# Performance work log

Measured on AMD Instinct MI355X. Metric: run time of the kernel, lower is better.

## Reference

```python
import jax, jax.numpy as jnp
import numpy as np
from jax import lax

DN = ('NCHW', 'OIHW', 'NCHW')
K = 7  # kernel_size


def _conv(x, w, pad):
    return lax.conv_general_dilated(x, w, (1, 1), pad, dimension_numbers=DN)


def _rgb2gray(im):
    if im.shape[1] == 3:
        w = jnp.array([0.299, 0.587, 0.114], im.dtype)
        return jnp.einsum('bchw,c->bhw', im, w)[:, None]
    return im


def _block_detect(x, y):
    gx_img = _rgb2gray(x)
    gy_img = _rgb2gray(y)
    sob_x = jnp.array([[-1., 0., 1.], [-2., 0., 2.], [-1., 0., 1.]], x.dtype).reshape(1, 1, 3, 3)
    sob_y = jnp.array([[-1., -2., -1.], [0., 0., 0.], [1., 2., 1.]], x.dtype).reshape(1, 1, 3, 3)
    pad = ((1, 1), (1, 1))
    in_gx = _conv(gx_img, sob_x, pad).at[:, :, :, -1].set(1.0)
    in_gy = _conv(gx_img, sob_y, pad).at[:, :, -1, :].set(1.0)
    rf_gx = _conv(gy_img, sob_x, pad).at[:, :, :, -1].set(1.0)
    rf_gy = _conv(gy_img, sob_y, pad).at[:, :, -1, :].set(1.0)
    n_in = jnp.sqrt(in_gx * in_gx + in_gy * in_gy)
    n_rf = jnp.sqrt(rf_gx * rf_gx + rf_gy * rf_gy)
    cos = (in_gx * rf_gx + in_gy * rf_gy + 0.001) / (n_in * n_rf + 0.001)
    one_m = 1.0 - cos
    sigma = (n_in >= 29.0).astype(x.dtype)
    theta = n_rf >= 29.0
    # cosxy ** theta with theta in {0,1}: where(theta, one_m, 1) is identical math with clean grads
    return sigma * jnp.where(theta, one_m, 1.0)


def _forward(x, y, w1, b1, w2, b2):
    k = K
    c = x.shape[1]
    ks = c * k * k  # 147 patch features
    eye_c = jnp.eye(ks, dtype=x.dtype).reshape(ks, c, k, k)   # one-hot im2col kernel (matches torch layout c,ky,kx)
    eye_1 = jnp.eye(k * k, dtype=x.dtype).reshape(k * k, 1, k, k)
    inp_p = _conv(x, eye_c, 'VALID')   # [B,ks,Nh,Nw]
    ref_p = _conv(y, eye_c, 'VALID')
    B, _, Nh, Nw = inp_p.shape
    N = Nh * Nw
    block = 1.0 - _block_detect(x, y)  # [B,1,H,W]
    blk_p = _conv(block, eye_1, 'VALID').mean(axis=1, keepdims=True).reshape(B, 1, N)  # sum/k^2
    # conv1: 1x1 convs 147->3 (ReLU) ->1, per-query bandwidth h
    h1 = jax.nn.relu(jnp.einsum('bchw,oc->bohw', ref_p, w1) + b1[None, :, None, None])
    h = (jnp.einsum('bchw,oc->bohw', h1, w2) + b2[None, :, None, None]).reshape(B, N, 1)
    Xr = ref_p.reshape(B, ks, N)
    XY = jnp.einsum('bkn,bkm->bnm', Xr, Xr)          # [B,N,N]
    sq = jnp.sum(Xr * Xr, axis=1)                    # [B,N] (== XX and YY, matrix is symmetric)
    att = (2.0 * XY - sq[:, :, None] - sq[:, None, :]) / (h * h + 1.0)
    att = jax.nn.softmax(att, axis=-1) * blk_p       # multiplicative block mask over keys
    att = att / (jnp.sum(att, axis=-1, keepdims=True) + 0.001)
    out_p = jnp.einsum('bnm,bkm->bkn', att, inp_p.reshape(B, ks, N)).reshape(B, ks, Nh, Nw)
    # img_sum: overlap-add fold == adjoint of the VALID im2col conv
    folded = lax.conv_transpose(out_p, eye_c, (1, 1), 'VALID', dimension_numbers=DN, transpose_kernel=True)
    wts = lax.conv_transpose(jnp.ones((1, k * k, Nh, Nw), x.dtype), eye_1, (1, 1), 'VALID',
                             dimension_numbers=DN, transpose_kernel=True)
    return folded / wts


def setup_inputs() -> dict:
    key = jax.random.key(0)
    k1, k2, k3, k4 = jax.random.split(key, 4)
    B, C, H, W = 2, 3, 63, 63  # H*W < min_size=6400 -> direct forward_chop path
    ks = C * K * K
    x = jax.random.uniform(k1, (B, C, H, W), jnp.float32) * 255.0
    y = jax.random.uniform(k2, (B, C, H, W), jnp.float32) * 255.0
    w1 = jax.random.normal(k3, (C, ks), jnp.float32) * 0.05
    b1 = jnp.zeros((C,), jnp.float32)
    w2 = jax.random.normal(k4, (1, C), jnp.float32) * 0.05
    b2 = jnp.zeros((1,), jnp.float32)
    return {"x": x, "y": y, "w1": w1, "b1": b1, "w2": w2, "b2": b2}


def reference(x, y, w1, b1, w2, b2):
    return _forward(x, y, w1, b1, w2, b2)
```

## Files before the change

kernel.cpp:

```cpp
#include <hip/hip_runtime.h>
#include <cstddef>

namespace nl {
constexpr int B = 2, C = 3, H = 63, W = 63, K = 7;
constexpr int NH = 57, NW = 57, N = NH * NW;
constexpr int KS = 147, KSP = 160, NPAD = 3328;
constexpr int SPLITS = 8;
constexpr int MCHUNK = NPAD / SPLITS;
constexpr int MSTEPS = MCHUNK / 32;
constexpr size_t SZ_X   = (size_t)B * KSP * NPAD;
constexpr size_t OFF_XR = 0;
constexpr size_t OFF_XIB = SZ_X;
constexpr size_t OFF_SQ = OFF_XIB + SZ_X / 2;
constexpr size_t OFF_HD = OFF_SQ + (size_t)B * NPAD;
constexpr size_t OFF_BLK = OFF_HD + (size_t)B * NPAD;
constexpr size_t OFF_DI = OFF_BLK + (size_t)B * NPAD;
constexpr size_t OFF_BIMG = OFF_DI + (size_t)B * NPAD;
constexpr size_t OFF_ATT = OFF_BIMG + 8192;
constexpr size_t SZ_ATT = (size_t)B * NPAD * NPAD;
constexpr size_t OFF_OUTA = OFF_ATT + SZ_ATT;
}
using namespace nl;

typedef __attribute__((ext_vector_type(8))) short short8;
typedef __attribute__((ext_vector_type(4))) float floatx4;

__device__ inline unsigned short f2bf(float f) {
  unsigned int u = __float_as_uint(f);
  unsigned int r = (u + 0x7FFFu + ((u >> 16) & 1u)) >> 16;
  return (unsigned short)r;
}

__global__ __launch_bounds__(256) void nl_block(const float* __restrict__ x,
                                                const float* __restrict__ y,
                                                float* __restrict__ bimg) {
  int idx = blockIdx.x * 256 + threadIdx.x;
  if (idx >= B * H * W) return;
  int q = idx % W, t = idx / W;
  int p = t % H, b = t / H;
  float gx[3][3], gy[3][3];
#pragma unroll
  for (int dy = 0; dy < 3; ++dy)
#pragma unroll
    for (int dx = 0; dx < 3; ++dx) {
      int pp = p + dy - 1, qq = q + dx - 1;
      float vx = 0.f, vy = 0.f;
      if (pp >= 0 && pp < H && qq >= 0 && qq < W) {
        int base = (b * C * H + pp) * W + qq;
        vx = 0.299f * x[base] + 0.587f * x[base + H * W] + 0.114f * x[base + 2 * H * W];
        vy = 0.299f * y[base] + 0.587f * y[base + H * W] + 0.114f * y[base + 2 * H * W];
      }
      gx[dy][dx] = vx; gy[dy][dx] = vy;
    }
  float in_gx = (q == W - 1) ? 1.f : (-gx[0][0] + gx[0][2] - 2.f * gx[1][0] + 2.f * gx[1][2] - gx[2][0] + gx[2][2]);
  float in_gy = (p == H - 1) ? 1.f : (-gx[0][0] - 2.f * gx[0][1] - gx[0][2] + gx[2][0] + 2.f * gx[2][1] + gx[2][2]);
  float rf_gx = (q == W - 1) ? 1.f : (-gy[0][0] + gy[0][2] - 2.f * gy[1][0] + 2.f * gy[1][2] - gy[2][0] + gy[2][2]);
  float rf_gy = (p == H - 1) ? 1.f : (-gy[0][0] - 2.f * gy[0][1] - gy[0][2] + gy[2][0] + 2.f * gy[2][1] + gy[2][2]);
  float n_in = sqrtf(in_gx * in_gx + in_gy * in_gy);
  float n_rf = sqrtf(rf_gx * rf_gx + rf_gy * rf_gy);
  float cosv = (in_gx * rf_gx + in_gy * rf_gy + 0.001f) / (n_in * n_rf + 0.001f);
  float det = (n_in >= 29.f) ? ((n_rf >= 29.f) ? (1.f - cosv) : 1.f) : 0.f;
  bimg[(b * H + p) * W + q] = 1.f - det;
}

__global__ __launch_bounds__(256) void nl_blkp(const float* __restrict__ bimg,
                                               float* __restrict__ blk) {
  int idx = blockIdx.x * 256 + threadIdx.x;
  if (idx >= B * NPAD) return;
  int n = idx % NPAD, b = idx / NPAD;
  float v = 0.f;
  if (n < N) {
    int i = n / NW, j = n % NW;
    float s = 0.f;
#pragma unroll
    for (int ky = 0; ky < K; ++ky)
#pragma unroll
      for (int kx = 0; kx < K; ++kx)
        s += bimg[(b * H + i + ky) * W + (j + kx)];
    v = s * (1.f / 49.f);
  }
  blk[idx] = v;
}

__global__ __launch_bounds__(256) void nl_im2col(const float* __restrict__ x,
                                                 const float* __restrict__ y,
                                                 float* __restrict__ ws) {
  size_t idx = (size_t)blockIdx.x * 256 + threadIdx.x;
  if (idx >= 2 * SZ_X) return;
  if (idx < SZ_X) {
    int n = (int)(idx % NPAD);
    int r1 = (int)(idx / NPAD);
    int k = r1 % KSP, b = r1 / KSP;
    float v = 0.f;
    if (k < KS && n < N) {
      int c = k / 49, r = k % 49;
      int ky = r / 7, kx = r % 7;
      int i = n / NW, j = n % NW;
      v = y[((b * C + c) * H + (i + ky)) * W + (j + kx)];
    }
    ws[OFF_XR + idx] = v;
  } else {
    size_t i2 = idx - SZ_X;
    int n = (int)(i2 % NPAD);
    int r1 = (int)(i2 / NPAD);
    int k = r1 % KSP, b = r1 / KSP;
    float v = 0.f;
    if (k < KS && n < N) {
      int c = k / 49, r = k % 49;
      int ky = r / 7, kx = r % 7;
      int i = n / NW, j = n % NW;
      v = x[((b * C + c) * H + (i + ky)) * W + (j + kx)];
    }
    ((unsigned short*)(ws + OFF_XIB))[i2] = f2bf(v);
  }
}

__global__ __launch_bounds__(256) void nl_sqh(const float* __restrict__ ws_xr,
                                              const float* __restrict__ w1,
                                              const float* __restrict__ b1,
                                              const float* __restrict__ w2,
                                              const float* __restrict__ b2,
                                              float* __restrict__ sq,
                                              float* __restrict__ hd) {
  int idx = blockIdx.x * 256 + threadIdx.x;
  if (idx >= B * NPAD) return;
  int n = idx % NPAD, b = idx / NPAD;
  if (n >= N) { sq[idx] = 0.f; hd[idx] = 1.f; return; }
  const float* Xr = ws_xr + (size_t)b * KSP * NPAD + n;
  float s = 0.f, h0 = b1[0], h1 = b1[1], h2 = b1[2];
  for (int k = 0; k < KS; ++k) {
    float v = Xr[(size_t)k * NPAD];
    s += v * v;
    h0 += v * w1[k];
    h1 += v * w1[KS + k];
    h2 += v * w1[2 * KS + k];
  }
  h0 = fmaxf(h0, 0.f); h1 = fmaxf(h1, 0.f); h2 = fmaxf(h2, 0.f);
  float h = h0 * w2[0] + h1 * w2[1] + h2 * w2[2] + b2[0];
  sq[idx] = s;
  hd[idx] = h * h + 1.f;
}

__global__ __launch_bounds__(256) void nl_gemm1(const float* __restrict__ ws_xr,
                                                const float* __restrict__ sq,
                                                const float* __restrict__ hd,
                                                float* __restrict__ att) {
  int bx = blockIdx.x, by = blockIdx.y;
  if (bx < by) return;
  __shared__ float As[32][128];
  __shared__ float Bs[32][128];
  int b = blockIdx.z;
  const float* Xb = ws_xr + (size_t)b * KSP * NPAD;
  int row0 = by * 128, col0 = bx * 128;
  int t = threadIdx.x;
  int tr = t >> 4, tc = t & 15;
  float acc[8][8];
#pragma unroll
  for (int i = 0; i < 8; ++i)
#pragma unroll
    for (int j = 0; j < 8; ++j) acc[i][j] = 0.f;

  for (int kt = 0; kt < KSP; kt += 32) {
#pragma unroll
    for (int u = 0; u < 4; ++u) {
      int e = t + u * 256;
      int kk = e >> 5, cc = e & 31;
      float4 va = *(const float4*)(Xb + (size_t)(kt + kk) * NPAD + row0 + cc * 4);
      *(float4*)(&As[kk][cc * 4]) = va;
      float4 vb = *(const float4*)(Xb + (size_t)(kt + kk) * NPAD + col0 + cc * 4);
      *(float4*)(&Bs[kk][cc * 4]) = vb;
    }
    __syncthreads();
#pragma unroll
    for (int kk = 0; kk < 32; ++kk) {
      float a[8], bb[8];
      *(float4*)(&a[0]) = *(const float4*)(&As[kk][tr * 4]);
      *(float4*)(&a[4]) = *(const float4*)(&As[kk][64 + tr * 4]);
      *(float4*)(&bb[0]) = *(const float4*)(&Bs[kk][tc * 4]);
      *(float4*)(&bb[4]) = *(const float4*)(&Bs[kk][64 + tc * 4]);
#pragma unroll
      for (int i = 0; i < 8; ++i)
#pragma unroll
        for (int j = 0; j < 8; ++j) acc[i][j] = fmaf(a[i], bb[j], acc[i][j]);
    }
    __syncthreads();
  }
  int rI[8], cJ[8];
#pragma unroll
  for (int i = 0; i < 4; ++i) { rI[i] = row0 + tr * 4 + i; rI[i + 4] = row0 + 64 + tr * 4 + i; }
#pragma unroll
  for (int j = 0; j < 4; ++j) { cJ[j] = col0 + tc * 4 + j; cJ[j + 4] = col0 + 64 + tc * 4 + j; }
  float sqn[8], hin[8], sqm[8], him[8];
#pragma unroll
  for (int i = 0; i < 8; ++i) { sqn[i] = sq[b * NPAD + rI[i]]; hin[i] = 1.f / hd[b * NPAD + rI[i]]; }
#pragma unroll
  for (int j = 0; j < 8; ++j) { sqm[j] = sq[b * NPAD + cJ[j]]; him[j] = 1.f / hd[b * NPAD + cJ[j]]; }
#pragma unroll
  for (int i = 0; i < 8; ++i) {
    float v[8];
#pragma unroll
    for (int j = 0; j < 8; ++j)
      v[j] = __expf((2.f * acc[i][j] - sqn[i] - sqm[j]) * hin[i]);
    float* arow = att + ((size_t)b * NPAD + rI[i]) * NPAD;
    *(float4*)(arow + col0 + tc * 4) = *(float4*)(&v[0]);
    *(float4*)(arow + col0 + 64 + tc * 4) = *(float4*)(&v[4]);
  }
  if (bx != by) {
#pragma unroll
    for (int j = 0; j < 8; ++j) {
      float v[8];
#pragma unroll
      for (int i = 0; i < 8; ++i)
        v[i] = __expf((2.f * acc[i][j] - sqn[i] - sqm[j]) * him[j]);
      float* arow = att + ((size_t)b * NPAD + cJ[j]) * NPAD;
      *(float4*)(arow + row0 + tr * 4) = *(float4*)(&v[0]);
      *(float4*)(arow + row0 + 64 + tr * 4) = *(float4*)(&v[4]);
    }
  }
}

__global__ __launch_bounds__(256) void nl_ssum(const float* __restrict__ att,
                                               const float* __restrict__ blk,
                                               float* __restrict__ dinv) {
  int n = blockIdx.x, b = blockIdx.y;
  int tid = threadIdx.x;
  if (n >= N) { if (tid == 0) dinv[b * NPAD + n] = 0.f; return; }
  const float* row = att + ((size_t)b * NPAD + n) * NPAD;
  const float* bl = blk + b * NPAD;
  float s1 = 0.f, s2 = 0.f;
  for (int m = tid; m < N; m += 256) {
    float e = row[m];
    s1 += e;
    s2 += e * bl[m];
  }
  __shared__ float r1[256], r2[256];
  r1[tid] = s1; r2[tid] = s2;
  __syncthreads();
  for (int s = 128; s > 0; s >>= 1) {
    if (tid < s) { r1[tid] += r1[tid + s]; r2[tid] += r2[tid + s]; }
    __syncthreads();
  }
  if (tid == 0) dinv[b * NPAD + n] = 1.f / (r2[0] + 0.001f * r1[0]);
}

__global__ __launch_bounds__(256) void nl_gemm2(const float* __restrict__ att,
                                                const unsigned short* __restrict__ xib,
                                                const float* __restrict__ dinv,
                                                const float* __restrict__ blk,
                                                float* __restrict__ outp0) {
  __shared__ unsigned short Plds[128][32];
  __shared__ unsigned short Xlds[160][32];
  __shared__ float dil[128];
  int b = blockIdx.z;
  int n0 = blockIdx.x * 128;
  int m0 = blockIdx.y * MCHUNK;
  const float* attb = att + (size_t)b * NPAD * NPAD;
  const unsigned short* Xib = xib + (size_t)b * KSP * NPAD;
  const float* blkb = blk + b * NPAD;
  int t = threadIdx.x;
  if (t < 128) dil[t] = dinv[b * NPAD + n0 + t];
  int lane = t & 63, wv = t >> 6;
  int li = lane & 15, lg = lane >> 4;
  int pq = t & 7, pn0 = t >> 3;

  floatx4 acc[2][10];
#pragma unroll
  for (int a = 0; a < 2; ++a)
#pragma unroll
    for (int j = 0; j < 10; ++j) acc[a][j] = (floatx4)0.f;

  float4 pa[4];
  ushort4 px[5];
  float4 bl4;
  bl4 = *(const float4*)(blkb + m0 + pq * 4);
#pragma unroll
  for (int u = 0; u < 4; ++u)
    pa[u] = *(const float4*)(attb + (size_t)(n0 + pn0 + u * 32) * NPAD + m0 + pq * 4);
#pragma unroll
  for (int u = 0; u < 5; ++u)
    px[u] = *(const ushort4*)(Xib + (size_t)(pn0 + u * 32) * NPAD + m0 + pq * 4);

  for (int it = 0; it < MSTEPS; ++it) {
    __syncthreads();
#pragma unroll
    for (int u = 0; u < 4; ++u) {
      ushort4 o;
      o.x = f2bf(pa[u].x * bl4.x);
      o.y = f2bf(pa[u].y * bl4.y);
      o.z = f2bf(pa[u].z * bl4.z);
      o.w = f2bf(pa[u].w * bl4.w);
      *(ushort4*)(&Plds[pn0 + u * 32][pq * 4]) = o;
    }
#pragma unroll
    for (int u = 0; u < 5; ++u)
      *(ushort4*)(&Xlds[pn0 + u * 32][pq * 4]) = px[u];
    __syncthreads();
    if (it + 1 < MSTEPS) {
      int mn = m0 + (it + 1) * 32;
      bl4 = *(const float4*)(blkb + mn + pq * 4);
#pragma unroll
      for (int u = 0; u < 4; ++u)
        pa[u] = *(const float4*)(attb + (size_t)(n0 + pn0 + u * 32) * NPAD + mn + pq * 4);
#pragma unroll
      for (int u = 0; u < 5; ++u)
        px[u] = *(const ushort4*)(Xib + (size_t)(pn0 + u * 32) * NPAD + mn + pq * 4);
    }
    short8 bf2[2];
#pragma unroll
    for (int a = 0; a < 2; ++a)
      bf2[a] = *(const short8*)(&Plds[32 * wv + 16 * a + li][8 * lg]);
#pragma unroll
    for (int j = 0; j < 10; ++j) {
      short8 af = *(const short8*)(&Xlds[16 * j + li][8 * lg]);
#pragma unroll
      for (int a = 0; a < 2; ++a)
        acc[a][j] = __builtin_amdgcn_mfma_f32_16x16x32_bf16(af, bf2[a], acc[a][j], 0, 0, 0);
    }
  }
  float* outp = outp0 + (size_t)b * KSP * NPAD;
#pragma unroll
  for (int a = 0; a < 2; ++a) {
    int nloc = 32 * wv + 16 * a + li;
    int n = n0 + nloc;
    float dv = dil[nloc];
#pragma unroll
    for (int j = 0; j < 10; ++j) {
#pragma unroll
      for (int r = 0; r < 4; ++r) {
        int k = 16 * j + 4 * lg + r;
        atomicAdd(outp + (size_t)k * NPAD + n, acc[a][j][r] * dv);
      }
    }
  }
}

__global__ __launch_bounds__(256) void nl_fold(const float* __restrict__ outA,
                                               float* __restrict__ out) {
  int idx = blockIdx.x * 256 + threadIdx.x;
  if (idx >= B * C * H * W) return;
  int q = idx % W, t = idx / W;
  int p = t % H, t2 = t / H;
  int c = t2 % C, b = t2 / C;
  float s = 0.f;
#pragma unroll
  for (int ky = 0; ky < K; ++ky) {
    int iy = p - ky;
    if (iy < 0 || iy >= NH) continue;
#pragma unroll
    for (int kx = 0; kx < K; ++kx) {
      int jx = q - kx;
      if (jx < 0 || jx >= NW) continue;
      size_t o = ((size_t)(b * KSP + c * 49 + ky * 7 + kx)) * NPAD + iy * NW + jx;
      s += outA[o];
    }
  }
  int cy = min(p, 6) - max(0, p - 56) + 1;
  int cx = min(q, 6) - max(0, q - 56) + 1;
  out[idx] = s / (float)(cy * cx);
}

extern "C" void kernel_launch(void* const* d_in, const int* in_sizes, int n_in,
                              void* d_out, int out_size, void* d_ws, size_t ws_size,
                              hipStream_t stream) {
  const float* x = (const float*)d_in[0];
  const float* y = (const float*)d_in[1];
  const float* w1 = (const float*)d_in[2];
  const float* b1 = (const float*)d_in[3];
  const float* w2 = (const float*)d_in[4];
  const float* b2 = (const float*)d_in[5];
  float* ws = (float*)d_ws;
  float* out = (float*)d_out;

  float* Xr = ws + OFF_XR;
  unsigned short* Xib = (unsigned short*)(ws + OFF_XIB);
  float* sq = ws + OFF_SQ;
  float* hd = ws + OFF_HD;
  float* blk = ws + OFF_BLK;
  float* dinv = ws + OFF_DI;
  float* bimg = ws + OFF_BIMG;
  float* att = ws + OFF_ATT;
  float* outA = ws + OFF_OUTA;

  hipMemsetAsync(outA, 0, SZ_X * sizeof(float), stream);

  nl_block<<<(B * H * W + 255) / 256, 256, 0, stream>>>(x, y, bimg);
  nl_im2col<<<(int)((2 * SZ_X + 255) / 256), 256, 0, stream>>>(x, y, ws);
  nl_blkp<<<(B * NPAD + 255) / 256, 256, 0, stream>>>(bimg, blk);
  nl_sqh<<<(B * NPAD + 255) / 256, 256, 0, stream>>>(Xr, w1, b1, w2, b2, sq, hd);
  nl_gemm1<<<dim3(NPAD / 128, NPAD / 128, B), 256, 0, stream>>>(Xr, sq, hd, att);
  nl_ssum<<<dim3(NPAD, B), 256, 0, stream>>>(att, blk, dinv);
  nl_gemm2<<<dim3(NPAD / 128, SPLITS, B), 256, 0, stream>>>(att, Xib, dinv, blk, outA);
  nl_fold<<<(B * C * H * W + 255) / 256, 256, 0, stream>>>(outA, out);
}
```

Measured before the change: 224.5 us.

## Store attention matrix in bf16, fold block weights into Xi, prefetch gemm1 tiles

Result: slower. 236.8 us (+5.5%).

```diff
diff --git a/kernel.cpp b/kernel.cpp
--- a/kernel.cpp
+++ b/kernel.cpp
@@ -18,17 +18,21 @@
 constexpr size_t OFF_BIMG = OFF_DI + (size_t)B * NPAD;
 constexpr size_t OFF_ATT = OFF_BIMG + 8192;
 constexpr size_t SZ_ATT = (size_t)B * NPAD * NPAD;
-constexpr size_t OFF_OUTA = OFF_ATT + SZ_ATT;
+constexpr size_t OFF_OUTA = OFF_ATT + SZ_ATT / 2;
 }
 using namespace nl;
 
 typedef __attribute__((ext_vector_type(8))) short short8;
+typedef __attribute__((ext_vector_type(8))) unsigned short ushort8;
 typedef __attribute__((ext_vector_type(4))) float floatx4;
 
 __device__ inline unsigned short f2bf(float f) {
   unsigned int u = __float_as_uint(f);
   unsigned int r = (u + 0x7FFFu + ((u >> 16) & 1u)) >> 16;
   return (unsigned short)r;
+}
+__device__ inline float bf2f(unsigned short s) {
+  return __uint_as_float(((unsigned int)s) << 16);
 }
 
 __global__ __launch_bounds__(256) void nl_block(const float* __restrict__ x,
@@ -84,6 +88,7 @@
 
 __global__ __launch_bounds__(256) void nl_im2col(const float* __restrict__ x,
                                                  const float* __restrict__ y,
+                                                 const float* __restrict__ blk,
                                                  float* __restrict__ ws) {
   size_t idx = (size_t)blockIdx.x * 256 + threadIdx.x;
   if (idx >= 2 * SZ_X) return;
@@ -109,7 +114,7 @@
       int c = k / 49, r = k % 49;
       int ky = r / 7, kx = r % 7;
       int i = n / NW, j = n % NW;
-      v = x[((b * C + c) * H + (i + ky)) * W + (j + kx)];
+      v = x[((b * C + c) * H + (i + ky)) * W + (j + kx)] * blk[b * NPAD + n];
     }
     ((unsigned short*)(ws + OFF_XIB))[i2] = f2bf(v);
   }
@@ -144,7 +149,7 @@
 __global__ __launch_bounds__(256) void nl_gemm1(const float* __restrict__ ws_xr,
                                                 const float* __restrict__ sq,
                                                 const float* __restrict__ hd,
-                                                float* __restrict__ att) {
+                                                unsigned short* __restrict__ att) {
   int bx = blockIdx.x, by = blockIdx.y;
   if (bx < by) return;
   __shared__ float As[32][128];
@@ -160,17 +165,33 @@
 #pragma unroll
     for (int j = 0; j < 8; ++j) acc[i][j] = 0.f;
 
+  float4 va[4], vb[4];
+#pragma unroll
+  for (int u = 0; u < 4; ++u) {
+    int e = t + u * 256;
+    int kk = e >> 5, cc = e & 31;
+    va[u] = *(const float4*)(Xb + (size_t)kk * NPAD + row0 + cc * 4);
+    vb[u] = *(const float4*)(Xb + (size_t)kk * NPAD + col0 + cc * 4);
+  }
   for (int kt = 0; kt < KSP; kt += 32) {
+    __syncthreads();
 #pragma unroll
     for (int u = 0; u < 4; ++u) {
       int e = t + u * 256;
       int kk = e >> 5, cc = e & 31;
-      float4 va = *(const float4*)(Xb + (size_t)(kt + kk) * NPAD + row0 + cc * 4);
-      *(float4*)(&As[kk][cc * 4]) = va;
-      float4 vb = *(const float4*)(Xb + (size_t)(kt + kk) * NPAD + col0 + cc * 4);
-      *(float4*)(&Bs[kk][cc * 4]) = vb;
+      *(float4*)(&As[kk][cc * 4]) = va[u];
+      *(float4*)(&Bs[kk][cc * 4]) = vb[u];
     }
     __syncthreads();
+    if (kt + 32 < KSP) {
+#pragma unroll
+      for (int u = 0; u < 4; ++u) {
+        int e = t + u * 256;
+        int kk = e >> 5, cc = e & 31;
+        va[u] = *(const float4*)(Xb + (size_t)(kt + 32 + kk) * NPAD + row0 + cc * 4);
+        vb[u] = *(const float4*)(Xb + (size_t)(kt + 32 + kk) * NPAD + col0 + cc * 4);
+      }
+    }
 #pragma unroll
     for (int kk = 0; kk < 32; ++kk) {
       float a[8], bb[8];
@@ -183,7 +204,6 @@
 #pragma unroll
         for (int j = 0; j < 8; ++j) acc[i][j] = fmaf(a[i], bb[j], acc[i][j]);
     }
-    __syncthreads();
   }
   int rI[8], cJ[8];
 #pragma unroll
@@ -197,41 +217,57 @@
   for (int j = 0; j < 8; ++j) { sqm[j] = sq[b * NPAD + cJ[j]]; him[j] = 1.f / hd[b * NPAD + cJ[j]]; }
 #pragma unroll
   for (int i = 0; i < 8; ++i) {
-    float v[8];
-#pragma unroll
-    for (int j = 0; j < 8; ++j)
-      v[j] = __expf((2.f * acc[i][j] - sqn[i] - sqm[j]) * hin[i]);
-    float* arow = att + ((size_t)b * NPAD + rI[i]) * NPAD;
-    *(float4*)(arow + col0 + tc * 4) = *(float4*)(&v[0]);
-    *(float4*)(arow + col0 + 64 + tc * 4) = *(float4*)(&v[4]);
+    ushort4 o0, o1;
+    o0.x = f2bf(__expf((2.f * acc[i][0] - sqn[i] - sqm[0]) * hin[i]));
+    o0.y = f2bf(__expf((2.f * acc[i][1] - sqn[i] - sqm[1]) * hin[i]));
+    o0.z = f2bf(__expf((2.f * acc[i][2] - sqn[i] - sqm[2]) * hin[i]));
+    o0.w = f2bf(__expf((2.f * acc[i][3] - sqn[i] - sqm[3]) * hin[i]));
+    o1.x = f2bf(__expf((2.f * acc[i][4] - sqn[i] - sqm[4]) * hin[i]));
+    o1.y = f2bf(__expf((2.f * acc[i][5] - sqn[i] - sqm[5]) * hin[i]));
+    o1.z = f2bf(__expf((2.f * acc[i][6] - sqn[i] - sqm[6]) * hin[i]));
+    o1.w = f2bf(__expf((2.f * acc[i][7] - sqn[i] - sqm[7]) * hin[i]));
+    unsigned short* arow = att + ((size_t)b * NPAD + rI[i]) * NPAD;
+    *(ushort4*)(arow + col0 + tc * 4) = o0;
+    *(ushort4*)(arow + col0 + 64 + tc * 4) = o1;
   }
   if (bx != by) {
 #pragma unroll
     for (int j = 0; j < 8; ++j) {
-      float v[8];
-#pragma unroll
-      for (int i = 0; i < 8; ++i)
-        v[i] = __expf((2.f * acc[i][j] - sqn[i] - sqm[j]) * him[j]);
-      float* arow = att + ((size_t)b * NPAD + cJ[j]) * NPAD;
-      *(float4*)(arow + row0 + tr * 4) = *(float4*)(&v[0]);
-      *(float4*)(arow + row0 + 64 + tr * 4) = *(float4*)(&v[4]);
-    }
-  }
-}
-
-__global__ __launch_bounds__(256) void nl_ssum(const float* __restrict__ att,
+      ushort4 o0, o1;
+      o0.x = f2bf(__expf((2.f * acc[0][j] - sqn[0] - sqm[j]) * him[j]));
+      o0.y = f2bf(__expf((2.f * acc[1][j] - sqn[1] - sqm[j]) * him[j]));
+      o0.z = f2bf(__expf((2.f * acc[2][j] - sqn[2] - sqm[j]) * him[j]));
+      o0.w = f2bf(__expf((2.f * acc[3][j] - sqn[3] - sqm[j]) * him[j]));
+      o1.x = f2bf(__expf((2.f * acc[4][j] - sqn[4] - sqm[j]) * him[j]));
+      o1.y = f2bf(__expf((2.f * acc[5][j] - sqn[5] - sqm[j]) * him[j]));
+      o1.z = f2bf(__expf((2.f * acc[6][j] - sqn[6] - sqm[j]) * him[j]));
+      o1.w = f2bf(__expf((2.f * acc[7][j] - sqn[7] - sqm[j]) * him[j]));
+      unsigned short* arow = att + ((size_t)b * NPAD + cJ[j]) * NPAD;
+      *(ushort4*)(arow + row0 + tr * 4) = o0;
+      *(ushort4*)(arow + row0 + 64 + tr * 4) = o1;
+    }
+  }
+}
+
+__global__ __launch_bounds__(256) void nl_ssum(const unsigned short* __restrict__ att,
                                                const float* __restrict__ blk,
                                                float* __restrict__ dinv) {
   int n = blockIdx.x, b = blockIdx.y;
   int tid = threadIdx.x;
   if (n >= N) { if (tid == 0) dinv[b * NPAD + n] = 0.f; return; }
-  const float* row = att + ((size_t)b * NPAD + n) * NPAD;
+  const unsigned short* row = att + ((size_t)b * NPAD + n) * NPAD;
   const float* bl = blk + b * NPAD;
   float s1 = 0.f, s2 = 0.f;
-  for (int m = tid; m < N; m += 256) {
-    float e = row[m];
-    s1 += e;
-    s2 += e * bl[m];
+  constexpr int NCH = (N + 7) / 8;
+  for (int m8 = tid; m8 < NCH; m8 += 256) {
+    ushort8 v = *(const ushort8*)(row + m8 * 8);
+#pragma unroll
+    for (int j = 0; j < 8; ++j) {
+      int m = m8 * 8 + j;
+      float e = bf2f(v[j]);
+      if (m < N) s1 += e;
+      s2 += e * bl[m];
+    }
   }
   __shared__ float r1[256], r2[256];
   r1[tid] = s1; r2[tid] = s2;
@@ -243,10 +279,9 @@
   if (tid == 0) dinv[b * NPAD + n] = 1.f / (r2[0] + 0.001f * r1[0]);
 }
 
-__global__ __launch_bounds__(256) void nl_gemm2(const float* __restrict__ att,
+__global__ __launch_bounds__(256) void nl_gemm2(const unsigned short* __restrict__ att,
                                                 const unsigned short* __restrict__ xib,
                                                 const float* __restrict__ dinv,
-                                                const float* __restrict__ blk,
                                                 float* __restrict__ outp0) {
   __shared__ unsigned short Plds[128][32];
   __shared__ unsigned short Xlds[160][32];
@@ -254,9 +289,8 @@
   int b = blockIdx.z;
   int n0 = blockIdx.x * 128;
   int m0 = blockIdx.y * MCHUNK;
-  const float* attb = att + (size_t)b * NPAD * NPAD;
+  const unsigned short* attb = att + (size_t)b * NPAD * NPAD;
   const unsigned short* Xib = xib + (size_t)b * KSP * NPAD;
-  const float* blkb = blk + b * NPAD;
   int t = threadIdx.x;
   if (t < 128) dil[t] = dinv[b * NPAD + n0 + t];
   int lane = t & 63, wv = t >> 6;
@@ -269,13 +303,10 @@
 #pragma unroll
     for (int j = 0; j < 10; ++j) acc[a][j] = (floatx4)0.f;
 
-  float4 pa[4];
-  ushort4 px[5];
-  float4 bl4;
-  bl4 = *(const float4*)(blkb + m0 + pq * 4);
+  ushort4 pa[4], px[5];
 #pragma unroll
   for (int u = 0; u < 4; ++u)
-    pa[u] = *(const float4*)(attb + (size_t)(n0 + pn0 + u * 32) * NPAD + m0 + pq * 4);
+    pa[u] = *(const ushort4*)(attb + (size_t)(n0 + pn0 + u * 32) * NPAD + m0 + pq * 4);
 #pragma unroll
   for (int u = 0; u < 5; ++u)
     px[u] = *(const ushort4*)(Xib + (size_t)(pn0 + u * 32) * NPAD + m0 + pq * 4);
@@ -283,24 +314,17 @@
   for (int it = 0; it < MSTEPS; ++it) {
     __syncthreads();
 #pragma unroll
-    for (int u = 0; u < 4; ++u) {
-      ushort4 o;
-      o.x = f2bf(pa[u].x * bl4.x);
-      o.y = f2bf(pa[u].y * bl4.y);
-      o.z = f2bf(pa[u].z * bl4.z);
-      o.w = f2bf(pa[u].w * bl4.w);
-      *(ushort4*)(&Plds[pn0 + u * 32][pq * 4]) = o;
-    }
+    for (int u = 0; u < 4; ++u)
+      *(ushort4*)(&Plds[pn0 + u * 32][pq * 4]) = pa[u];
 #pragma unroll
     for (int u = 0; u < 5; ++u)
       *(ushort4*)(&Xlds[pn0 + u * 32][pq * 4]) = px[u];
     __syncthreads();
     if (it + 1 < MSTEPS) {
       int mn = m0 + (it + 1) * 32;
-      bl4 = *(const float4*)(blkb + mn + pq * 4);
 #pragma unroll
       for (int u = 0; u < 4; ++u)
-        pa[u] = *(const float4*)(attb + (size_t)(n0 + pn0 + u * 32) * NPAD + mn + pq * 4);
+        pa[u] = *(const ushort4*)(attb + (size_t)(n0 + pn0 + u * 32) * NPAD + mn + pq * 4);
 #pragma unroll
       for (int u = 0; u < 5; ++u)
         px[u] = *(const ushort4*)(Xib + (size_t)(pn0 + u * 32) * NPAD + mn + pq * 4);
@@ -378,17 +402,17 @@
   float* blk = ws + OFF_BLK;
   float* dinv = ws + OFF_DI;
   float* bimg = ws + OFF_BIMG;
-  float* att = ws + OFF_ATT;
+  unsigned short* att = (unsigned short*)(ws + OFF_ATT);
   float* outA = ws + OFF_OUTA;
 
   hipMemsetAsync(outA, 0, SZ_X * sizeof(float), stream);
 
   nl_block<<<(B * H * W + 255) / 256, 256, 0, stream>>>(x, y, bimg);
-  nl_im2col<<<(int)((2 * SZ_X + 255) / 256), 256, 0, stream>>>(x, y, ws);
   nl_blkp<<<(B * NPAD + 255) / 256, 256, 0, stream>>>(bimg, blk);
+  nl_im2col<<<(int)((2 * SZ_X + 255) / 256), 256, 0, stream>>>(x, y, blk, ws);
   nl_sqh<<<(B * NPAD + 255) / 256, 256, 0, stream>>>(Xr, w1, b1, w2, b2, sq, hd);
   nl_gemm1<<<dim3(NPAD / 128, NPAD / 128, B), 256, 0, stream>>>(Xr, sq, hd, att);
   nl_ssum<<<dim3(NPAD, B), 256, 0, stream>>>(att, blk, dinv);
-  nl_gemm2<<<dim3(NPAD / 128, SPLITS, B), 256, 0, stream>>>(att, Xib, dinv, blk, outA);
+  nl_gemm2<<<dim3(NPAD / 128, SPLITS, B), 256, 0, stream>>>(att, Xib, dinv, outA);
   nl_fold<<<(B * C * H * W + 255) / 256, 256, 0, stream>>>(outA, out);
 }
```
